# Performance work log

Measured on AMD Instinct MI355X. Metric: run time of the kernel, lower is better.

## Reference

```python
import jax, jax.numpy as jnp
import numpy as np

EMBED_DIM = 1024
N_HEADS = 16
HEAD_DIM = EMBED_DIM // N_HEADS  # 64
ROPE_DIM = 4
N_FREQ = HEAD_DIM // (2 * ROPE_DIM)  # 8 rotary freqs per coordinate axis
ROPE_THETA = 10000.0
FFN_DIM = 4 * EMBED_DIM
N_TOK = 4096
N_SEQ = 8
EPS = 1e-5
NEG_INF = -1e30


def setup_inputs() -> dict:
    key = jax.random.key(0)
    ks = jax.random.split(key, 16)
    s = 0.02
    coords = jax.random.uniform(ks[0], (N_TOK, ROPE_DIM), jnp.float32) * 10.0
    feats = jax.random.normal(ks[1], (N_TOK, EMBED_DIM), jnp.float32)
    interior = jnp.sort(jax.random.randint(ks[2], (N_SEQ - 1,), 1, N_TOK)).astype(jnp.int32)
    cu_seqlens = jnp.concatenate([jnp.zeros((1,), jnp.int32), interior,
                                  jnp.full((1,), N_TOK, jnp.int32)])
    # learnable RoPE inverse frequencies, one bank per coordinate axis
    base = 1.0 / (ROPE_THETA ** (jnp.arange(N_FREQ, dtype=jnp.float32) * 2.0 * ROPE_DIM / HEAD_DIM))
    inv_freq = jnp.tile(base[None, :], (ROPE_DIM, 1))  # [rope_dim, n_freq]
    return {
        "coords": coords,
        "feats": feats,
        "cu_seqlens": cu_seqlens,
        "Wqkv": jax.random.normal(ks[3], (EMBED_DIM, 3 * EMBED_DIM), jnp.float32) * s,
        "bqkv": jnp.zeros((3 * EMBED_DIM,), jnp.float32),
        "Wo": jax.random.normal(ks[4], (EMBED_DIM, EMBED_DIM), jnp.float32) * s,
        "bo": jnp.zeros((EMBED_DIM,), jnp.float32),
        "inv_freq": inv_freq,
        "ln1_g": jnp.ones((EMBED_DIM,), jnp.float32),
        "ln1_b": jnp.zeros((EMBED_DIM,), jnp.float32),
        "W1": jax.random.normal(ks[5], (EMBED_DIM, FFN_DIM), jnp.float32) * s,
        "b1": jnp.zeros((FFN_DIM,), jnp.float32),
        "W2": jax.random.normal(ks[6], (FFN_DIM, EMBED_DIM), jnp.float32) * s,
        "b2": jnp.zeros((EMBED_DIM,), jnp.float32),
        "ln2_g": jnp.ones((EMBED_DIM,), jnp.float32),
        "ln2_b": jnp.zeros((EMBED_DIM,), jnp.float32),
    }


def _layernorm(x, g, b):
    mu = jnp.mean(x, axis=-1, keepdims=True)
    xc = x - mu
    var = jnp.mean(xc * xc, axis=-1, keepdims=True)
    return xc * jax.lax.rsqrt(var + EPS) * g + b


def _block_forward(coords, feats, cu_seqlens, Wqkv, bqkv, Wo, bo, inv_freq,
                   ln1_g, ln1_b, W1, b1, W2, b2, ln2_g, ln2_b):
    N, D = feats.shape
    qkv = (feats @ Wqkv + bqkv).reshape(N, 3, N_HEADS, HEAD_DIM)
    q, k, v = qkv[:, 0], qkv[:, 1], qkv[:, 2]  # each [N, H, hd]

    # multi-dimensional learnable RoPE: each coord axis rotates its freq bank
    ang = jnp.einsum('nd,df->ndf', coords, inv_freq).reshape(N, 1, HEAD_DIM // 2)
    cos, sin = jnp.cos(ang), jnp.sin(ang)

    def rot(x):
        x1, x2 = jnp.split(x, 2, axis=-1)
        return jnp.concatenate([x1 * cos - x2 * sin, x2 * cos + x1 * sin], axis=-1)

    q, k = rot(q), rot(k)

    # varlen block-diagonal attention mask from cu_seqlens
    seg = jnp.searchsorted(cu_seqlens[1:], jnp.arange(N), side='right')
    mask = seg[:, None] == seg[None, :]  # [N, N]

    scores = jnp.einsum('nhd,mhd->hnm', q, k) / np.sqrt(HEAD_DIM).astype(np.float32)
    scores = jnp.where(mask[None, :, :], scores, NEG_INF)
    attn = jax.nn.softmax(scores, axis=-1)
    o = jnp.einsum('hnm,mhd->nhd', attn, v).reshape(N, D) @ Wo + bo

    h = _layernorm(feats + o, ln1_g, ln1_b)
    f = jax.nn.gelu(h @ W1 + b1) @ W2 + b2
    return _layernorm(h + f, ln2_g, ln2_b)


def reference(coords, feats, cu_seqlens, Wqkv, bqkv, Wo, bo, inv_freq,
              ln1_g, ln1_b, W1, b1, W2, b2, ln2_g, ln2_b):
    return _block_forward(coords, feats, cu_seqlens, Wqkv, bqkv, Wo, bo, inv_freq,
                          ln1_g, ln1_b, W1, b1, W2, b2, ln2_g, ln2_b)
```

## Files before the change

kernel.cpp:

```cpp
#include <hip/hip_runtime.h>

#define NTOK 4096
#define EMB  1024
#define NH   16
#define HD   64
#define FFN  4096

typedef __bf16 bf16x8 __attribute__((ext_vector_type(8)));
typedef float  f32x4  __attribute__((ext_vector_type(4)));

#define ASG __attribute__((address_space(1)))
#define ASL __attribute__((address_space(3)))

__device__ __forceinline__ float b2f(unsigned short u) {
    union { unsigned int i; float f; } v; v.i = ((unsigned int)u) << 16; return v.f;
}
__device__ __forceinline__ unsigned short f2b(float f) {
    union { float f; unsigned int i; } v; v.f = f;
    unsigned int x = v.i;
    return (unsigned short)((x + 0x7fffu + ((x >> 16) & 1u)) >> 16);
}
__device__ __forceinline__ float ldf(const void* p, size_t i, int f32) {
    return f32 ? ((const float*)p)[i] : b2f(((const unsigned short*)p)[i]);
}
__device__ __forceinline__ int probe_f32(const void* p) {
    return ((const unsigned int*)p)[0] == 0x3F800000u ? 1 : 0;
}
__device__ __forceinline__ float gelu_f(float x) {
    float z = 0.7978845608028654f * (x + 0.044715f * x * x * x);
    float t = 1.0f - 2.0f / (__expf(2.0f * z) + 1.0f);
    return 0.5f * x * (1.0f + t);
}
__device__ __forceinline__ void gll16(const void* g, void* l) {
    __builtin_amdgcn_global_load_lds((const ASG void*)g, (ASL void*)l, 16, 0, 0);
}

__global__ __launch_bounds__(256) void convert_kernel(
    const void* __restrict__ feats, const void* __restrict__ bqkv,
    const void* __restrict__ bo, const void* __restrict__ b1,
    const void* __restrict__ b2, const void* __restrict__ g1,
    const void* __restrict__ e1, const void* __restrict__ g2,
    const void* __restrict__ e2, const int* __restrict__ cu,
    unsigned short* __restrict__ feats_bf, unsigned short* __restrict__ smalls,
    int* __restrict__ seg, const void* __restrict__ pr) {
    const int f32 = probe_f32(pr);
    int bid = blockIdx.x, tid = threadIdx.x;
    if (bid < 4096) {
        size_t base = (size_t)bid * 1024 + tid * 4;
        union { unsigned short u[4]; int2 v; } U;
#pragma unroll
        for (int i = 0; i < 4; ++i) U.u[i] = f2b(ldf(feats, base + i, f32));
        *reinterpret_cast<int2*>(&feats_bf[base]) = U.v;
    } else if (bid < 4109) {
        int flat = (bid - 4096) * 1024 + tid * 4;
        const void* src; int off;
        if      (flat < 3072)  { src = bqkv; off = 0; }
        else if (flat < 4096)  { src = bo;   off = 3072; }
        else if (flat < 8192)  { src = b1;   off = 4096; }
        else if (flat < 9216)  { src = b2;   off = 8192; }
        else if (flat < 10240) { src = g1;   off = 9216; }
        else if (flat < 11264) { src = e1;   off = 10240; }
        else if (flat < 12288) { src = g2;   off = 11264; }
        else                   { src = e2;   off = 12288; }
        union { unsigned short u[4]; int2 v; } U;
#pragma unroll
        for (int i = 0; i < 4; ++i) U.u[i] = f2b(ldf(src, flat - off + i, f32));
        *reinterpret_cast<int2*>(&smalls[flat]) = U.v;
    } else {
        int n = (bid - 4109) * 256 + tid;
        int s = 0;
#pragma unroll
        for (int i = 1; i <= 8; ++i) s += (cu[i] <= n) ? 1 : 0;
        seg[n] = s;
    }
}

__global__ __launch_bounds__(256) void transpose_kernel(
    const void* __restrict__ W, unsigned short* __restrict__ O,
    int K, int N, const void* __restrict__ pr) {
    const int f32 = probe_f32(pr);
    int b = blockIdx.x, tid = threadIdx.x;
    int ntiles = N >> 5;
    int nt = b % ntiles, kt = b / ntiles;
    __shared__ unsigned short T[32][33];
    int x = tid & 31, y = tid >> 5;
#pragma unroll
    for (int i = 0; i < 4; ++i) {
        int k = kt * 32 + y + 8 * i, n = nt * 32 + x;
        T[y + 8 * i][x] = f2b(ldf(W, (size_t)k * N + n, f32));
    }
    __syncthreads();
#pragma unroll
    for (int i = 0; i < 4; ++i) {
        int n = nt * 32 + y + 8 * i, k = kt * 32 + x;
        O[(size_t)n * K + k] = T[x][y + 8 * i];
    }
}

template <int ACT, int OUTEXT, int TN>
__global__ __launch_bounds__(256) void gemm128(
    const unsigned short* __restrict__ A, const unsigned short* __restrict__ Bt,
    const unsigned short* __restrict__ bias, void* __restrict__ C,
    int M, int N, int K, int lda, int ldb, const void* __restrict__ pr) {
    constexpr int NB = TN / 32;
    __shared__ __align__(16) unsigned short As[128 * 64];
    __shared__ __align__(16) unsigned short Bs[TN * 64];
    const int f32 = OUTEXT ? probe_f32(pr) : 0;
    const int tid = threadIdx.x;
    const int wave = tid >> 6, lane = tid & 63;
    const int wy = wave >> 1, wx = wave & 1;
    const int qm = lane & 15, quad = lane >> 4;
    int bx, by;
    if ((gridDim.y & 7) == 0) {
        int lin = blockIdx.y * gridDim.x + blockIdx.x;
        int ypg = gridDim.y >> 3;
        int xcd = lin & 7, s = lin >> 3;
        int sy = s / gridDim.x;
        by = xcd * ypg + sy;
        bx = s - sy * gridDim.x;
    } else { bx = blockIdx.x; by = blockIdx.y; }
    const int m0 = by * 128, n0 = bx * TN;
    const int r = lane >> 3, gl = lane & 7;

    f32x4 acc[4][NB];
#pragma unroll
    for (int i = 0; i < 4; ++i)
#pragma unroll
        for (int j = 0; j < NB; ++j) acc[i][j] = (f32x4){0.f, 0.f, 0.f, 0.f};

    const unsigned short* Ab = A  + (size_t)m0 * lda;
    const unsigned short* Bb = Bt + (size_t)n0 * ldb;

    for (int k0 = 0; k0 < K; k0 += 64) {
#pragma unroll
        for (int i = 0; i < 4; ++i) {
            int cc = wave * 4 + i;
            gll16(Ab + (size_t)(8 * cc + r) * lda + k0 + ((gl ^ r) << 3), &As[cc * 512]);
        }
#pragma unroll
        for (int i = 0; i < NB; ++i) {
            int cc = wave * NB + i;
            gll16(Bb + (size_t)(8 * cc + r) * ldb + k0 + ((gl ^ r) << 3), &Bs[cc * 512]);
        }
        __syncthreads();
#pragma unroll
        for (int h = 0; h < 2; ++h) {
            bf16x8 af[4], bfr[NB];
#pragma unroll
            for (int i = 0; i < 4; ++i) {
                int phys = (((h * 4 + quad) ^ (qm & 7)) << 3);
                af[i] = *reinterpret_cast<const bf16x8*>(&As[(64 * wy + 16 * i + qm) * 64 + phys]);
            }
#pragma unroll
            for (int j = 0; j < NB; ++j) {
                int phys = (((h * 4 + quad) ^ (qm & 7)) << 3);
                bfr[j] = *reinterpret_cast<const bf16x8*>(&Bs[((TN / 2) * wx + 16 * j + qm) * 64 + phys]);
            }
#pragma unroll
            for (int i = 0; i < 4; ++i)
#pragma unroll
                for (int j = 0; j < NB; ++j)
                    acc[i][j] = __builtin_amdgcn_mfma_f32_16x16x32_bf16(af[i], bfr[j], acc[i][j], 0, 0, 0);
        }
        __syncthreads();
    }
#pragma unroll
    for (int j = 0; j < NB; ++j) {
        int col = n0 + (TN / 2) * wx + 16 * j + qm;
        float bv = b2f(bias[col]);
#pragma unroll
        for (int i = 0; i < 4; ++i) {
            int rowb = m0 + 64 * wy + 16 * i + quad * 4;
#pragma unroll
            for (int rr = 0; rr < 4; ++rr) {
                size_t idx = (size_t)(rowb + rr) * N + col;
                float v = acc[i][j][rr] + bv;
                if (ACT == 1) v = gelu_f(v);
                if (OUTEXT && f32) ((float*)C)[idx] = v;
                else               ((unsigned short*)C)[idx] = f2b(v);
            }
        }
    }
}

__global__ __launch_bounds__(256) void rope_kernel(
    const void* __restrict__ coords, const void* __restrict__ inv_freq,
    unsigned short* __restrict__ qkv, const void* __restrict__ pr) {
    const int f32 = probe_f32(pr);
    int n = blockIdx.x, tid = threadIdx.x;
#pragma unroll
    for (int it = 0; it < 2; ++it) {
        int idx = tid + it * 256;
        int hh = idx >> 5, f = idx & 31;
        float c  = ldf(coords, n * 4 + (f >> 3), f32);
        float iv = ldf(inv_freq, f, f32);
        float sn, cs;
        sincosf(c * iv, &sn, &cs);
#pragma unroll
        for (int w = 0; w < 2; ++w) {
            size_t base = (size_t)n * 3072 + (size_t)w * 1024 + hh * 64;
            float x1 = b2f(qkv[base + f]);
            float x2 = b2f(qkv[base + 32 + f]);
            qkv[base + f]      = f2b(x1 * cs - x2 * sn);
            qkv[base + 32 + f] = f2b(x2 * cs + x1 * sn);
        }
    }
}

__global__ __launch_bounds__(256) void attn_part(
    const unsigned short* __restrict__ qkv, const int* __restrict__ seg,
    const int* __restrict__ cu, unsigned short* __restrict__ u0,
    unsigned short* __restrict__ u1, float* __restrict__ ml) {
    const int h  = blockIdx.y;
    const int piece = blockIdx.x & 1;
    const int t0 = (blockIdx.x >> 1) * 64;
    const int tid  = threadIdx.x;
    const int wave = tid >> 6, lane = tid & 63;
    const int qm = lane & 15, quad = lane >> 4;

    __shared__ __align__(16) unsigned short Ks[64][72];
    __shared__ __align__(16) unsigned short Ps[64][72];
    __shared__ __align__(16) unsigned short Vt[64 * 64];
    __shared__ int segq[64], segk[64];

    const unsigned short* qrow = qkv + (size_t)(t0 + 16 * wave + qm) * 3072 + h * 64;
    bf16x8 af0 = *reinterpret_cast<const bf16x8*>(qrow + quad * 8);
    bf16x8 af1 = *reinterpret_cast<const bf16x8*>(qrow + 32 + quad * 8);

    if (tid < 64) segq[tid] = seg[t0 + tid];
    __syncthreads();

    const int kbegT = cu[segq[0]];
    const int kendT = cu[segq[63] + 1];
    const int nchunks = (kendT - kbegT + 63) >> 6;
    const int half = (nchunks + 1) >> 1;
    const int kb = kbegT + (piece ? half * 64 : 0);
    const int ke = piece ? kendT : min(kendT, kbegT + half * 64);

    int sqr[4];
#pragma unroll
    for (int r = 0; r < 4; ++r) sqr[r] = segq[16 * wave + quad * 4 + r];
    const int wsmin = segq[16 * wave];
    const int wsmax = segq[16 * wave + 15];

    float m[4], l[4];
    f32x4 o[4];
#pragma unroll
    for (int r = 0; r < 4; ++r) { m[r] = -1e30f; l[r] = 0.0f; }
#pragma unroll
    for (int t = 0; t < 4; ++t) o[t] = (f32x4){0.f, 0.f, 0.f, 0.f};

    const int jrow = tid >> 2, dcol = (tid & 3) * 16;
    int4 kA, kB, vA, vB; int sg;
#define LOAD_CHUNK(KC)                                                          \
    {                                                                           \
        int kk = (KC) + jrow;                                                   \
        bool valid = kk < ke;                                                   \
        const unsigned short* kvb = qkv + (size_t)kk * 3072 + h * 64 + dcol;    \
        kA = valid ? *reinterpret_cast<const int4*>(kvb + 1024)     : (int4){0,0,0,0}; \
        kB = valid ? *reinterpret_cast<const int4*>(kvb + 1024 + 8) : (int4){0,0,0,0}; \
        vA = valid ? *reinterpret_cast<const int4*>(kvb + 2048)     : (int4){0,0,0,0}; \
        vB = valid ? *reinterpret_cast<const int4*>(kvb + 2048 + 8) : (int4){0,0,0,0}; \
        sg = 127;                                                               \
        if (tid < 64 && (KC) + tid < ke) sg = seg[(KC) + tid];                  \
    }

    if (kb < ke) LOAD_CHUNK(kb);

    for (int kc = kb; kc < ke; kc += 64) {
        __syncthreads();
        *reinterpret_cast<int4*>(&Ks[jrow][dcol])     = kA;
        *reinterpret_cast<int4*>(&Ks[jrow][dcol + 8]) = kB;
        {
            union { int4 v; unsigned short u[8]; } U0, U1;
            U0.v = vA; U1.v = vB;
            int g = jrow >> 3, jl = jrow & 7;
#pragma unroll
            for (int i = 0; i < 16; ++i) {
                int d = dcol + i;
                int phys = g ^ (d & 7) ^ ((d >> 3) & 7);
                Vt[d * 64 + phys * 8 + jl] = (i < 8) ? U0.u[i] : U1.u[i - 8];
            }
        }
        if (tid < 64) segk[tid] = sg;
        __syncthreads();

        if (kc + 64 < ke) LOAD_CHUNK(kc + 64);

        const int skmin = segk[0], skmax = segk[63];
        const bool act = !(skmax < wsmin || skmin > wsmax);

        if (act) {
            f32x4 sc[4];
#pragma unroll
            for (int nb = 0; nb < 4; ++nb) {
                bf16x8 bf0 = *reinterpret_cast<const bf16x8*>(&Ks[16 * nb + qm][quad * 8]);
                bf16x8 bf1 = *reinterpret_cast<const bf16x8*>(&Ks[16 * nb + qm][32 + quad * 8]);
                f32x4 s = (f32x4){0.f, 0.f, 0.f, 0.f};
                s = __builtin_amdgcn_mfma_f32_16x16x32_bf16(af0, bf0, s, 0, 0, 0);
                s = __builtin_amdgcn_mfma_f32_16x16x32_bf16(af1, bf1, s, 0, 0, 0);
                sc[nb] = s;
            }
#pragma unroll
            for (int nb = 0; nb < 4; ++nb) {
                int sk = segk[16 * nb + qm];
#pragma unroll
                for (int r = 0; r < 4; ++r)
                    sc[nb][r] = (sk == sqr[r]) ? sc[nb][r] * 0.125f : -1e30f;
            }
            float alpha[4];
#pragma unroll
            for (int r = 0; r < 4; ++r) {
                float v = fmaxf(fmaxf(sc[0][r], sc[1][r]), fmaxf(sc[2][r], sc[3][r]));
                v = fmaxf(v, __shfl_xor(v, 1, 64));
                v = fmaxf(v, __shfl_xor(v, 2, 64));
                v = fmaxf(v, __shfl_xor(v, 4, 64));
                v = fmaxf(v, __shfl_xor(v, 8, 64));
                float mn = fmaxf(m[r], v);
                alpha[r] = __expf(m[r] - mn);
                m[r] = mn;
            }
            float rs[4] = {0.f, 0.f, 0.f, 0.f};
#pragma unroll
            for (int nb = 0; nb < 4; ++nb)
#pragma unroll
                for (int r = 0; r < 4; ++r) {
                    float p = __expf(sc[nb][r] - m[r]);
                    sc[nb][r] = p;
                    rs[r] += p;
                }
#pragma unroll
            for (int r = 0; r < 4; ++r) {
                float v = rs[r];
                v += __shfl_xor(v, 1, 64);
                v += __shfl_xor(v, 2, 64);
                v += __shfl_xor(v, 4, 64);
                v += __shfl_xor(v, 8, 64);
                l[r] = l[r] * alpha[r] + v;
            }
#pragma unroll
            for (int nb = 0; nb < 4; ++nb)
#pragma unroll
                for (int r = 0; r < 4; ++r)
                    Ps[16 * wave + quad * 4 + r][16 * nb + qm] = f2b(sc[nb][r]);
#pragma unroll
            for (int t = 0; t < 4; ++t)
#pragma unroll
                for (int r = 0; r < 4; ++r) o[t][r] *= alpha[r];
        }
        __syncthreads();
        if (act) {
            bf16x8 pa0 = *reinterpret_cast<const bf16x8*>(&Ps[16 * wave + qm][quad * 8]);
            bf16x8 pa1 = *reinterpret_cast<const bf16x8*>(&Ps[16 * wave + qm][32 + quad * 8]);
#pragma unroll
            for (int dt = 0; dt < 4; ++dt) {
                int row = 16 * dt + qm;
                int base = ((row >> 3) & 7) ^ (row & 7);
                bf16x8 vb0 = *reinterpret_cast<const bf16x8*>(&Vt[row * 64 + ((quad ^ base) << 3)]);
                bf16x8 vb1 = *reinterpret_cast<const bf16x8*>(&Vt[row * 64 + (((4 + quad) ^ base) << 3)]);
                o[dt] = __builtin_amdgcn_mfma_f32_16x16x32_bf16(pa0, vb0, o[dt], 0, 0, 0);
                o[dt] = __builtin_amdgcn_mfma_f32_16x16x32_bf16(pa1, vb1, o[dt], 0, 0, 0);
            }
        }
    }
#undef LOAD_CHUNK
    unsigned short* dst = piece ? u1 : u0;
#pragma unroll
    for (int dt = 0; dt < 4; ++dt)
#pragma unroll
        for (int r = 0; r < 4; ++r) {
            int row = t0 + 16 * wave + quad * 4 + r;
            dst[(size_t)row * 1024 + h * 64 + 16 * dt + qm] = f2b(o[dt][r]);
        }
    if (qm == 0) {
        float2* ML = (float2*)ml;
#pragma unroll
        for (int r = 0; r < 4; ++r) {
            int row = t0 + 16 * wave + quad * 4 + r;
            ML[((piece * 16 + h) << 12) + row] = make_float2(m[r], l[r]);
        }
    }
}

__global__ __launch_bounds__(256) void combine_kernel(
    const unsigned short* __restrict__ u1, const float* __restrict__ ml,
    unsigned short* __restrict__ u0out) {
    int n = blockIdx.x, tid = threadIdx.x;
    int d4 = tid * 4, h = tid >> 4;
    const float2* ML = (const float2*)ml;
    float2 p0 = ML[(h << 12) + n];
    float2 p1 = ML[((16 + h) << 12) + n];
    float M = fmaxf(p0.x, p1.x);
    float a0 = __expf(p0.x - M), a1 = __expf(p1.x - M);
    float rcp = 1.0f / (a0 * p0.y + a1 * p1.y);
    size_t ix = (size_t)n * 1024 + d4;
    union { int2 q; unsigned short u[4]; } A, B, R;
    A.q = *reinterpret_cast<const int2*>(u0out + ix);
    B.q = *reinterpret_cast<const int2*>(u1 + ix);
#pragma unroll
    for (int i = 0; i < 4; ++i)
        R.u[i] = f2b((a0 * b2f(A.u[i]) + a1 * b2f(B.u[i])) * rcp);
    *reinterpret_cast<int2*>(u0out + ix) = R.q;
}

template <int X2EXT, int OUTEXT>
__global__ __launch_bounds__(256) void ln_kernel(
    const unsigned short* __restrict__ x1, const void* __restrict__ x2,
    const unsigned short* __restrict__ g, const unsigned short* __restrict__ b,
    void* __restrict__ out, const void* __restrict__ pr) {
    const int f32 = probe_f32(pr);
    int n = blockIdx.x, tid = threadIdx.x;
    __shared__ float red[8];
    const int d0 = tid * 4;
    const size_t ix0 = (size_t)n * EMB + d0;
    float v[4];
    {
        union { int2 q; unsigned short u[4]; } A;
        A.q = *reinterpret_cast<const int2*>(&x1[ix0]);
        if (X2EXT && f32) {
            float4 B = *reinterpret_cast<const float4*>((const float*)x2 + ix0);
            v[0] = b2f(A.u[0]) + B.x; v[1] = b2f(A.u[1]) + B.y;
            v[2] = b2f(A.u[2]) + B.z; v[3] = b2f(A.u[3]) + B.w;
        } else {
            union { int2 q; unsigned short u[4]; } B;
            B.q = *reinterpret_cast<const int2*>((const unsigned short*)x2 + ix0);
#pragma unroll
            for (int i = 0; i < 4; ++i) v[i] = b2f(A.u[i]) + b2f(B.u[i]);
        }
    }
    float s = v[0] + v[1] + v[2] + v[3];
#pragma unroll
    for (int off = 1; off < 64; off <<= 1) s += __shfl_xor(s, off, 64);
    if ((tid & 63) == 0) red[tid >> 6] = s;
    __syncthreads();
    float mu = (red[0] + red[1] + red[2] + red[3]) * (1.0f / 1024.0f);
    float sq = 0.0f;
#pragma unroll
    for (int i = 0; i < 4; ++i) { float c = v[i] - mu; sq += c * c; }
#pragma unroll
    for (int off = 1; off < 64; off <<= 1) sq += __shfl_xor(sq, off, 64);
    if ((tid & 63) == 0) red[4 + (tid >> 6)] = sq;
    __syncthreads();
    float var = (red[4] + red[5] + red[6] + red[7]) * (1.0f / 1024.0f);
    float rcp = rsqrtf(var + 1e-5f);
    union { int2 q; unsigned short u[4]; } G, Bb;
    G.q  = *reinterpret_cast<const int2*>(&g[d0]);
    Bb.q = *reinterpret_cast<const int2*>(&b[d0]);
    if (OUTEXT && f32) {
        float4 R;
        R.x = (v[0] - mu) * rcp * b2f(G.u[0]) + b2f(Bb.u[0]);
        R.y = (v[1] - mu) * rcp * b2f(G.u[1]) + b2f(Bb.u[1]);
        R.z = (v[2] - mu) * rcp * b2f(G.u[2]) + b2f(Bb.u[2]);
        R.w = (v[3] - mu) * rcp * b2f(G.u[3]) + b2f(Bb.u[3]);
        *reinterpret_cast<float4*>((float*)out + ix0) = R;
    } else {
        union { int2 q; unsigned short u[4]; } R;
#pragma unroll
        for (int i = 0; i < 4; ++i)
            R.u[i] = f2b((v[i] - mu) * rcp * b2f(G.u[i]) + b2f(Bb.u[i]));
        *reinterpret_cast<int2*>((unsigned short*)out + ix0) = R.q;
    }
}

extern "C" void kernel_launch(void* const* d_in, const int* in_sizes, int n_in,
                              void* d_out, int out_size, void* d_ws, size_t ws_size,
                              hipStream_t stream) {
    const void* coords   = d_in[0];
    const void* feats    = d_in[1];
    const int*  cu       = (const int*)d_in[2];
    const void* Wqkv     = d_in[3];
    const void* bqkv     = d_in[4];
    const void* Wo       = d_in[5];
    const void* bo       = d_in[6];
    const void* inv_freq = d_in[7];
    const void* ln1_g    = d_in[8];
    const void* ln1_b    = d_in[9];
    const void* W1       = d_in[10];
    const void* b1       = d_in[11];
    const void* W2       = d_in[12];
    const void* b2       = d_in[13];
    const void* ln2_g    = d_in[14];
    const void* ln2_b    = d_in[15];
    const void* pr = ln1_g;

    char* ws = (char*)d_ws;
    int* seg = (int*)ws;
    unsigned short* smalls   = (unsigned short*)(ws + 16384);
    unsigned short* bqkv_bf  = smalls;
    unsigned short* bo_bf    = smalls + 3072;
    unsigned short* b1_bf    = smalls + 4096;
    unsigned short* b2_bf    = smalls + 8192;
    unsigned short* g1_bf    = smalls + 9216;
    unsigned short* e1_bf    = smalls + 10240;
    unsigned short* g2_bf    = smalls + 11264;
    unsigned short* e2_bf    = smalls + 12288;
    unsigned short* feats_bf = (unsigned short*)(ws + 65536);
    unsigned short* hbuf     = feats_bf;
    unsigned short* W1_t     = (unsigned short*)(ws + 8454144);
    unsigned short* u1buf    = (unsigned short*)(ws + 16842752);
    unsigned short* Wqkv_t   = (unsigned short*)(ws + 18939904);
    unsigned short* qkv      = (unsigned short*)(ws + 25231360);
    unsigned short* attn_o   = (unsigned short*)(ws + 50397184);
    unsigned short* Wo_t     = (unsigned short*)(ws + 18939904);
    unsigned short* W2_t     = (unsigned short*)(ws + 16842752);
    unsigned short* proj     = (unsigned short*)(ws + 25231360);
    unsigned short* f1       = (unsigned short*)(ws + 25231360);
    float* mlbuf = (float*)d_out;

    hipLaunchKernelGGL(convert_kernel, dim3(4125), dim3(256), 0, stream,
                       feats, bqkv, bo, b1, b2, ln1_g, ln1_b, ln2_g, ln2_b, cu,
                       feats_bf, smalls, seg, pr);
    hipLaunchKernelGGL(transpose_kernel, dim3(3072), dim3(256), 0, stream,
                       Wqkv, Wqkv_t, 1024, 3072, pr);
    hipLaunchKernelGGL(transpose_kernel, dim3(4096), dim3(256), 0, stream,
                       W1, W1_t, 1024, 4096, pr);
    hipLaunchKernelGGL((gemm128<0, 0, 128>), dim3(24, 32), dim3(256), 0, stream,
                       feats_bf, Wqkv_t, bqkv_bf, qkv, NTOK, 3072, 1024, 1024, 1024, pr);
    hipLaunchKernelGGL(rope_kernel, dim3(NTOK), dim3(256), 0, stream,
                       coords, inv_freq, qkv, pr);
    hipLaunchKernelGGL(attn_part, dim3(128, NH), dim3(256), 0, stream,
                       qkv, seg, cu, attn_o, u1buf, mlbuf);
    hipLaunchKernelGGL(combine_kernel, dim3(NTOK), dim3(256), 0, stream,
                       u1buf, mlbuf, attn_o);
    hipLaunchKernelGGL(transpose_kernel, dim3(1024), dim3(256), 0, stream,
                       Wo, Wo_t, 1024, 1024, pr);
    hipLaunchKernelGGL((gemm128<0, 0, 64>), dim3(16, 32), dim3(256), 0, stream,
                       attn_o, Wo_t, bo_bf, proj, NTOK, 1024, 1024, 1024, 1024, pr);
    hipLaunchKernelGGL(transpose_kernel, dim3(4096), dim3(256), 0, stream,
                       W2, W2_t, 4096, 1024, pr);
    hipLaunchKernelGGL((ln_kernel<0, 0>), dim3(NTOK), dim3(256), 0, stream,
                       feats_bf, proj, g1_bf, e1_bf, hbuf, pr);
    hipLaunchKernelGGL((gemm128<1, 0, 128>), dim3(32, 32), dim3(256), 0, stream,
                       hbuf, W1_t, b1_bf, f1, NTOK, 4096, 1024, 1024, 1024, pr);
    hipLaunchKernelGGL((gemm128<0, 1, 64>), dim3(16, 32), dim3(256), 0, stream,
                       f1, W2_t, b2_bf, d_out, NTOK, 1024, 4096, 4096, 4096, pr);
    hipLaunchKernelGGL((ln_kernel<1, 1>), dim3(NTOK), dim3(256), 0, stream,
                       hbuf, d_out, g2_bf, e2_bf, d_out, pr);
}
```

Before: 448.8 us.

## Write V transposed from QKV GEMM and split attention into three KV pieces

The QKV GEMM epilogue now writes Q/K into a compact 2048-wide buffer and V pre-transposed (d-major), so attention loads V rows directly into LDS without the per-element swizzled transpose. The softmax scale moves into the rope kernel, and masking is skipped when a chunk lies in a single segment. Attention also splits each query tile's KV range into three pieces instead of two for more parallelism, with a three-way combine. Dropping the key-validity guard on loads relies on the aligned range staying in bounds, a barrier is removed, and f2b now uses a hardware bf16 convert.

```diff
diff --git a/kernel.cpp b/kernel.cpp
--- a/kernel.cpp
+++ b/kernel.cpp
@@ -16,9 +16,7 @@
     union { unsigned int i; float f; } v; v.i = ((unsigned int)u) << 16; return v.f;
 }
 __device__ __forceinline__ unsigned short f2b(float f) {
-    union { float f; unsigned int i; } v; v.f = f;
-    unsigned int x = v.i;
-    return (unsigned short)((x + 0x7fffu + ((x >> 16) & 1u)) >> 16);
+    return __builtin_bit_cast(unsigned short, (__bf16)f);
 }
 __device__ __forceinline__ float ldf(const void* p, size_t i, int f32) {
     return f32 ? ((const float*)p)[i] : b2f(((const unsigned short*)p)[i]);
@@ -97,10 +95,11 @@
     }
 }
 
-template <int ACT, int OUTEXT, int TN>
+template <int ACT, int OUTEXT, int TN, int SPLITV>
 __global__ __launch_bounds__(256) void gemm128(
     const unsigned short* __restrict__ A, const unsigned short* __restrict__ Bt,
     const unsigned short* __restrict__ bias, void* __restrict__ C,
+    void* __restrict__ C2,
     int M, int N, int K, int lda, int ldb, const void* __restrict__ pr) {
     constexpr int NB = TN / 32;
     __shared__ __align__(16) unsigned short As[128 * 64];
@@ -168,16 +167,29 @@
     for (int j = 0; j < NB; ++j) {
         int col = n0 + (TN / 2) * wx + 16 * j + qm;
         float bv = b2f(bias[col]);
-#pragma unroll
-        for (int i = 0; i < 4; ++i) {
-            int rowb = m0 + 64 * wy + 16 * i + quad * 4;
-#pragma unroll
-            for (int rr = 0; rr < 4; ++rr) {
-                size_t idx = (size_t)(rowb + rr) * N + col;
-                float v = acc[i][j][rr] + bv;
-                if (ACT == 1) v = gelu_f(v);
-                if (OUTEXT && f32) ((float*)C)[idx] = v;
-                else               ((unsigned short*)C)[idx] = f2b(v);
+        if (SPLITV && n0 >= 2048) {
+            int d = col - 2048;
+#pragma unroll
+            for (int i = 0; i < 4; ++i) {
+                int rowb = m0 + 64 * wy + 16 * i + quad * 4;
+                union { unsigned short u[4]; int2 v; } U;
+#pragma unroll
+                for (int rr = 0; rr < 4; ++rr) U.u[rr] = f2b(acc[i][j][rr] + bv);
+                *reinterpret_cast<int2*>((unsigned short*)C2 + (size_t)d * 4096 + rowb) = U.v;
+            }
+        } else {
+            const int ldc = SPLITV ? 2048 : N;
+#pragma unroll
+            for (int i = 0; i < 4; ++i) {
+                int rowb = m0 + 64 * wy + 16 * i + quad * 4;
+#pragma unroll
+                for (int rr = 0; rr < 4; ++rr) {
+                    size_t idx = (size_t)(rowb + rr) * ldc + col;
+                    float v = acc[i][j][rr] + bv;
+                    if (ACT == 1) v = gelu_f(v);
+                    if (OUTEXT && f32) ((float*)C)[idx] = v;
+                    else               ((unsigned short*)C)[idx] = f2b(v);
+                }
             }
         }
     }
@@ -185,7 +197,7 @@
 
 __global__ __launch_bounds__(256) void rope_kernel(
     const void* __restrict__ coords, const void* __restrict__ inv_freq,
-    unsigned short* __restrict__ qkv, const void* __restrict__ pr) {
+    unsigned short* __restrict__ qk, const void* __restrict__ pr) {
     const int f32 = probe_f32(pr);
     int n = blockIdx.x, tid = threadIdx.x;
 #pragma unroll
@@ -198,44 +210,47 @@
         sincosf(c * iv, &sn, &cs);
 #pragma unroll
         for (int w = 0; w < 2; ++w) {
-            size_t base = (size_t)n * 3072 + (size_t)w * 1024 + hh * 64;
-            float x1 = b2f(qkv[base + f]);
-            float x2 = b2f(qkv[base + 32 + f]);
-            qkv[base + f]      = f2b(x1 * cs - x2 * sn);
-            qkv[base + 32 + f] = f2b(x2 * cs + x1 * sn);
+            size_t base = (size_t)n * 2048 + (size_t)w * 1024 + hh * 64;
+            float scl = w ? 1.0f : 0.125f;
+            float x1 = b2f(qk[base + f]);
+            float x2 = b2f(qk[base + 32 + f]);
+            qk[base + f]      = f2b((x1 * cs - x2 * sn) * scl);
+            qk[base + 32 + f] = f2b((x2 * cs + x1 * sn) * scl);
         }
     }
 }
 
 __global__ __launch_bounds__(256) void attn_part(
-    const unsigned short* __restrict__ qkv, const int* __restrict__ seg,
-    const int* __restrict__ cu, unsigned short* __restrict__ u0,
-    unsigned short* __restrict__ u1, float* __restrict__ ml) {
+    const unsigned short* __restrict__ qk, const unsigned short* __restrict__ vt,
+    const int* __restrict__ seg, const int* __restrict__ cu,
+    unsigned short* __restrict__ u0, unsigned short* __restrict__ u1,
+    unsigned short* __restrict__ u2, float* __restrict__ ml) {
     const int h  = blockIdx.y;
-    const int piece = blockIdx.x & 1;
-    const int t0 = (blockIdx.x >> 1) * 64;
+    const int t3 = blockIdx.x / 3;
+    const int piece = blockIdx.x - 3 * t3;
+    const int t0 = t3 * 64;
     const int tid  = threadIdx.x;
     const int wave = tid >> 6, lane = tid & 63;
     const int qm = lane & 15, quad = lane >> 4;
 
     __shared__ __align__(16) unsigned short Ks[64][72];
-    __shared__ __align__(16) unsigned short Ps[64][72];
-    __shared__ __align__(16) unsigned short Vt[64 * 64];
+    __shared__ __align__(16) unsigned short Vs[64][72];
+    __shared__ __align__(16) unsigned short Ps[64][76];
     __shared__ int segq[64], segk[64];
 
-    const unsigned short* qrow = qkv + (size_t)(t0 + 16 * wave + qm) * 3072 + h * 64;
+    const unsigned short* qrow = qk + (size_t)(t0 + 16 * wave + qm) * 2048 + h * 64;
     bf16x8 af0 = *reinterpret_cast<const bf16x8*>(qrow + quad * 8);
     bf16x8 af1 = *reinterpret_cast<const bf16x8*>(qrow + 32 + quad * 8);
 
     if (tid < 64) segq[tid] = seg[t0 + tid];
     __syncthreads();
 
-    const int kbegT = cu[segq[0]];
+    const int kbegA = cu[segq[0]] & ~63;
     const int kendT = cu[segq[63] + 1];
-    const int nchunks = (kendT - kbegT + 63) >> 6;
-    const int half = (nchunks + 1) >> 1;
-    const int kb = kbegT + (piece ? half * 64 : 0);
-    const int ke = piece ? kendT : min(kendT, kbegT + half * 64);
+    const int nchunks = (kendT - kbegA + 63) >> 6;
+    const int third = (nchunks + 2) / 3;
+    const int kb = kbegA + piece * third * 64;
+    const int ke = min(kendT, kbegA + (piece + 1) * third * 64);
 
     int sqr[4];
 #pragma unroll
@@ -250,38 +265,28 @@
 #pragma unroll
     for (int t = 0; t < 4; ++t) o[t] = (f32x4){0.f, 0.f, 0.f, 0.f};
 
-    const int jrow = tid >> 2, dcol = (tid & 3) * 16;
+    const int krow = tid >> 2, kdc = (tid & 3) * 16;
     int4 kA, kB, vA, vB; int sg;
-#define LOAD_CHUNK(KC)                                                          \
-    {                                                                           \
-        int kk = (KC) + jrow;                                                   \
-        bool valid = kk < ke;                                                   \
-        const unsigned short* kvb = qkv + (size_t)kk * 3072 + h * 64 + dcol;    \
-        kA = valid ? *reinterpret_cast<const int4*>(kvb + 1024)     : (int4){0,0,0,0}; \
-        kB = valid ? *reinterpret_cast<const int4*>(kvb + 1024 + 8) : (int4){0,0,0,0}; \
-        vA = valid ? *reinterpret_cast<const int4*>(kvb + 2048)     : (int4){0,0,0,0}; \
-        vB = valid ? *reinterpret_cast<const int4*>(kvb + 2048 + 8) : (int4){0,0,0,0}; \
-        sg = 127;                                                               \
-        if (tid < 64 && (KC) + tid < ke) sg = seg[(KC) + tid];                  \
+#define LOAD_CHUNK(KC)                                                                   \
+    {                                                                                    \
+        const unsigned short* kp = qk + (size_t)((KC) + krow) * 2048 + 1024 + h * 64 + kdc; \
+        kA = *reinterpret_cast<const int4*>(kp);                                         \
+        kB = *reinterpret_cast<const int4*>(kp + 8);                                     \
+        const unsigned short* vp = vt + (size_t)(h * 64 + krow) * 4096 + (KC) + kdc;     \
+        vA = *reinterpret_cast<const int4*>(vp);                                         \
+        vB = *reinterpret_cast<const int4*>(vp + 8);                                     \
+        sg = 127;                                                                        \
+        if (tid < 64 && (KC) + tid < ke) sg = seg[(KC) + tid];                           \
     }
 
     if (kb < ke) LOAD_CHUNK(kb);
 
     for (int kc = kb; kc < ke; kc += 64) {
         __syncthreads();
-        *reinterpret_cast<int4*>(&Ks[jrow][dcol])     = kA;
-        *reinterpret_cast<int4*>(&Ks[jrow][dcol + 8]) = kB;
-        {
-            union { int4 v; unsigned short u[8]; } U0, U1;
-            U0.v = vA; U1.v = vB;
-            int g = jrow >> 3, jl = jrow & 7;
-#pragma unroll
-            for (int i = 0; i < 16; ++i) {
-                int d = dcol + i;
-                int phys = g ^ (d & 7) ^ ((d >> 3) & 7);
-                Vt[d * 64 + phys * 8 + jl] = (i < 8) ? U0.u[i] : U1.u[i - 8];
-            }
-        }
+        *reinterpret_cast<int4*>(&Ks[krow][kdc])     = kA;
+        *reinterpret_cast<int4*>(&Ks[krow][kdc + 8]) = kB;
+        *reinterpret_cast<int4*>(&Vs[krow][kdc])     = vA;
+        *reinterpret_cast<int4*>(&Vs[krow][kdc + 8]) = vB;
         if (tid < 64) segk[tid] = sg;
         __syncthreads();
 
@@ -301,12 +306,14 @@
                 s = __builtin_amdgcn_mfma_f32_16x16x32_bf16(af1, bf1, s, 0, 0, 0);
                 sc[nb] = s;
             }
-#pragma unroll
-            for (int nb = 0; nb < 4; ++nb) {
-                int sk = segk[16 * nb + qm];
-#pragma unroll
-                for (int r = 0; r < 4; ++r)
-                    sc[nb][r] = (sk == sqr[r]) ? sc[nb][r] * 0.125f : -1e30f;
+            if (!((skmin == skmax) & (wsmin == wsmax))) {
+#pragma unroll
+                for (int nb = 0; nb < 4; ++nb) {
+                    int sk = segk[16 * nb + qm];
+#pragma unroll
+                    for (int r = 0; r < 4; ++r)
+                        sc[nb][r] = (sk == sqr[r]) ? sc[nb][r] : -1e30f;
+                }
             }
             float alpha[4];
 #pragma unroll
@@ -347,24 +354,20 @@
             for (int t = 0; t < 4; ++t)
 #pragma unroll
                 for (int r = 0; r < 4; ++r) o[t][r] *= alpha[r];
-        }
-        __syncthreads();
-        if (act) {
+
             bf16x8 pa0 = *reinterpret_cast<const bf16x8*>(&Ps[16 * wave + qm][quad * 8]);
             bf16x8 pa1 = *reinterpret_cast<const bf16x8*>(&Ps[16 * wave + qm][32 + quad * 8]);
 #pragma unroll
             for (int dt = 0; dt < 4; ++dt) {
-                int row = 16 * dt + qm;
-                int base = ((row >> 3) & 7) ^ (row & 7);
-                bf16x8 vb0 = *reinterpret_cast<const bf16x8*>(&Vt[row * 64 + ((quad ^ base) << 3)]);
-                bf16x8 vb1 = *reinterpret_cast<const bf16x8*>(&Vt[row * 64 + (((4 + quad) ^ base) << 3)]);
+                bf16x8 vb0 = *reinterpret_cast<const bf16x8*>(&Vs[16 * dt + qm][quad * 8]);
+                bf16x8 vb1 = *reinterpret_cast<const bf16x8*>(&Vs[16 * dt + qm][32 + quad * 8]);
                 o[dt] = __builtin_amdgcn_mfma_f32_16x16x32_bf16(pa0, vb0, o[dt], 0, 0, 0);
                 o[dt] = __builtin_amdgcn_mfma_f32_16x16x32_bf16(pa1, vb1, o[dt], 0, 0, 0);
             }
         }
     }
 #undef LOAD_CHUNK
-    unsigned short* dst = piece ? u1 : u0;
+    unsigned short* dst = (piece == 0) ? u0 : ((piece == 1) ? u1 : u2);
 #pragma unroll
     for (int dt = 0; dt < 4; ++dt)
 #pragma unroll
@@ -383,23 +386,25 @@
 }
 
 __global__ __launch_bounds__(256) void combine_kernel(
-    const unsigned short* __restrict__ u1, const float* __restrict__ ml,
-    unsigned short* __restrict__ u0out) {
+    const unsigned short* __restrict__ u1, const unsigned short* __restrict__ u2,
+    const float* __restrict__ ml, unsigned short* __restrict__ u0out) {
     int n = blockIdx.x, tid = threadIdx.x;
     int d4 = tid * 4, h = tid >> 4;
     const float2* ML = (const float2*)ml;
     float2 p0 = ML[(h << 12) + n];
     float2 p1 = ML[((16 + h) << 12) + n];
-    float M = fmaxf(p0.x, p1.x);
-    float a0 = __expf(p0.x - M), a1 = __expf(p1.x - M);
-    float rcp = 1.0f / (a0 * p0.y + a1 * p1.y);
+    float2 p2 = ML[((32 + h) << 12) + n];
+    float M = fmaxf(p0.x, fmaxf(p1.x, p2.x));
+    float a0 = __expf(p0.x - M), a1 = __expf(p1.x - M), a2 = __expf(p2.x - M);
+    float rcp = 1.0f / (a0 * p0.y + a1 * p1.y + a2 * p2.y);
     size_t ix = (size_t)n * 1024 + d4;
-    union { int2 q; unsigned short u[4]; } A, B, R;
-    A.q = *reinterpret_cast<const int2*>(u0out + ix);
-    B.q = *reinterpret_cast<const int2*>(u1 + ix);
+    union { int2 q; unsigned short u[4]; } A, B, Cq, R;
+    A.q  = *reinterpret_cast<const int2*>(u0out + ix);
+    B.q  = *reinterpret_cast<const int2*>(u1 + ix);
+    Cq.q = *reinterpret_cast<const int2*>(u2 + ix);
 #pragma unroll
     for (int i = 0; i < 4; ++i)
-        R.u[i] = f2b((a0 * b2f(A.u[i]) + a1 * b2f(B.u[i])) * rcp);
+        R.u[i] = f2b((a0 * b2f(A.u[i]) + a1 * b2f(B.u[i]) + a2 * b2f(Cq.u[i])) * rcp);
     *reinterpret_cast<int2*>(u0out + ix) = R.q;
 }
 
@@ -499,13 +504,15 @@
     unsigned short* W1_t     = (unsigned short*)(ws + 8454144);
     unsigned short* u1buf    = (unsigned short*)(ws + 16842752);
     unsigned short* Wqkv_t   = (unsigned short*)(ws + 18939904);
-    unsigned short* qkv      = (unsigned short*)(ws + 25231360);
+    unsigned short* qkbuf    = (unsigned short*)(ws + 25231360);
+    unsigned short* vtbuf    = (unsigned short*)(ws + 42008576);
     unsigned short* attn_o   = (unsigned short*)(ws + 50397184);
     unsigned short* Wo_t     = (unsigned short*)(ws + 18939904);
     unsigned short* W2_t     = (unsigned short*)(ws + 16842752);
     unsigned short* proj     = (unsigned short*)(ws + 25231360);
     unsigned short* f1       = (unsigned short*)(ws + 25231360);
     float* mlbuf = (float*)d_out;
+    unsigned short* u2buf = (unsigned short*)((char*)d_out + 2097152);
 
     hipLaunchKernelGGL(convert_kernel, dim3(4125), dim3(256), 0, stream,
                        feats, bqkv, bo, b1, b2, ln1_g, ln1_b, ln2_g, ln2_b, cu,
@@ -514,26 +521,26 @@
                        Wqkv, Wqkv_t, 1024, 3072, pr);
     hipLaunchKernelGGL(transpose_kernel, dim3(4096), dim3(256), 0, stream,
                        W1, W1_t, 1024, 4096, pr);
-    hipLaunchKernelGGL((gemm128<0, 0, 128>), dim3(24, 32), dim3(256), 0, stream,
-                       feats_bf, Wqkv_t, bqkv_bf, qkv, NTOK, 3072, 1024, 1024, 1024, pr);
+    hipLaunchKernelGGL((gemm128<0, 0, 128, 1>), dim3(24, 32), dim3(256), 0, stream,
+                       feats_bf, Wqkv_t, bqkv_bf, qkbuf, vtbuf, NTOK, 3072, 1024, 1024, 1024, pr);
     hipLaunchKernelGGL(rope_kernel, dim3(NTOK), dim3(256), 0, stream,
-                       coords, inv_freq, qkv, pr);
-    hipLaunchKernelGGL(attn_part, dim3(128, NH), dim3(256), 0, stream,
-                       qkv, seg, cu, attn_o, u1buf, mlbuf);
+                       coords, inv_freq, qkbuf, pr);
+    hipLaunchKernelGGL(attn_part, dim3(192, NH), dim3(256), 0, stream,
+                       qkbuf, vtbuf, seg, cu, attn_o, u1buf, u2buf, mlbuf);
     hipLaunchKernelGGL(combine_kernel, dim3(NTOK), dim3(256), 0, stream,
-                       u1buf, mlbuf, attn_o);
+                       u1buf, u2buf, mlbuf, attn_o);
     hipLaunchKernelGGL(transpose_kernel, dim3(1024), dim3(256), 0, stream,
                        Wo, Wo_t, 1024, 1024, pr);
-    hipLaunchKernelGGL((gemm128<0, 0, 64>), dim3(16, 32), dim3(256), 0, stream,
-                       attn_o, Wo_t, bo_bf, proj, NTOK, 1024, 1024, 1024, 1024, pr);
+    hipLaunchKernelGGL((gemm128<0, 0, 64, 0>), dim3(16, 32), dim3(256), 0, stream,
+                       attn_o, Wo_t, bo_bf, proj, nullptr, NTOK, 1024, 1024, 1024, 1024, pr);
     hipLaunchKernelGGL(transpose_kernel, dim3(4096), dim3(256), 0, stream,
                        W2, W2_t, 4096, 1024, pr);
     hipLaunchKernelGGL((ln_kernel<0, 0>), dim3(NTOK), dim3(256), 0, stream,
                        feats_bf, proj, g1_bf, e1_bf, hbuf, pr);
-    hipLaunchKernelGGL((gemm128<1, 0, 128>), dim3(32, 32), dim3(256), 0, stream,
-                       hbuf, W1_t, b1_bf, f1, NTOK, 4096, 1024, 1024, 1024, pr);
-    hipLaunchKernelGGL((gemm128<0, 1, 64>), dim3(16, 32), dim3(256), 0, stream,
-                       f1, W2_t, b2_bf, d_out, NTOK, 1024, 4096, 4096, 4096, pr);
+    hipLaunchKernelGGL((gemm128<1, 0, 128, 0>), dim3(32, 32), dim3(256), 0, stream,
+                       hbuf, W1_t, b1_bf, f1, nullptr, NTOK, 4096, 1024, 1024, 1024, pr);
+    hipLaunchKernelGGL((gemm128<0, 1, 64, 0>), dim3(16, 32), dim3(256), 0, stream,
+                       f1, W2_t, b2_bf, d_out, nullptr, NTOK, 1024, 4096, 4096, 4096, pr);
     hipLaunchKernelGGL((ln_kernel<1, 1>), dim3(NTOK), dim3(256), 0, stream,
                        hbuf, d_out, g2_bf, e2_bf, d_out, pr);
 }
```

New measurement: 425.1 us. -5.3%, faster.
